# Performance work log

Hardware: AMD Instinct MI355X
Metric: run time of the kernel (lower is better)

## Reference

```python
import jax, jax.numpy as jnp
import numpy as np

N = 50000      # nodes (src = dst at both layers)
E = 800000     # edges per layer
T = 8          # time steps
C_IN = 16      # input channels
HID = 16       # conv1 out channels (hardcoded in SAGENet)
C_OUT = 32     # final out channels


def setup_inputs() -> dict:
    key = jax.random.key(0)
    ks = jax.random.split(key, 10)
    X = jax.random.normal(ks[0], (T, N, C_IN), dtype=jnp.float32)
    edge_index0 = jax.random.randint(ks[1], (2, E), 0, N, dtype=jnp.int32)
    edge_weight0 = jax.random.uniform(ks[2], (E,), dtype=jnp.float32)
    edge_index1 = jax.random.randint(ks[3], (2, E), 0, N, dtype=jnp.int32)
    edge_weight1 = jax.random.uniform(ks[4], (E,), dtype=jnp.float32)
    res_n_id0 = jnp.arange(N, dtype=jnp.int32)
    res_n_id1 = jnp.arange(N, dtype=jnp.int32)
    W1 = jax.random.normal(ks[5], (2 * C_IN, HID), dtype=jnp.float32) * 0.1
    b1 = jax.random.normal(ks[6], (HID,), dtype=jnp.float32) * 0.1
    W2 = jax.random.normal(ks[7], (2 * HID, C_OUT), dtype=jnp.float32) * 0.1
    b2 = jax.random.normal(ks[8], (C_OUT,), dtype=jnp.float32) * 0.1
    return {"X": X, "edge_index0": edge_index0, "edge_weight0": edge_weight0,
            "edge_index1": edge_index1, "edge_weight1": edge_weight1,
            "res_n_id0": res_n_id0, "res_n_id1": res_n_id1,
            "W1": W1, "b1": b1, "W2": W2, "b2": b2}


def sage_conv(x, edge_index, edge_weight, res_n_id, num_dst, W, b):
    # x: [N_src, T, C]; message = edge_weight * x[src]; mean-aggregate to dst;
    # concat residual x[res_n_id] then linear (old PyG SAGEConv, concat=True).
    src, dst = edge_index[0], edge_index[1]
    msg = x[src] * edge_weight[:, None, None]                      # [E, T, C]
    summed = jax.ops.segment_sum(msg, dst, num_segments=num_dst)   # [Nd, T, C]
    cnt = jax.ops.segment_sum(jnp.ones_like(edge_weight), dst, num_segments=num_dst)
    aggr = summed / jnp.maximum(cnt, 1.0)[:, None, None]
    h = jnp.concatenate([x[res_n_id], aggr], axis=-1)              # [Nd, T, 2C]
    return jnp.einsum('ntc,cd->ntd', h, W) + b


def reference(X, edge_index0, edge_weight0, edge_index1, edge_weight1,
              res_n_id0, res_n_id1, W1, b1, W2, b2):
    x = jnp.transpose(X, (1, 0, 2))                                # [N, T, C]
    x = jax.nn.leaky_relu(sage_conv(x, edge_index0, edge_weight0, res_n_id0, N, W1, b1), 0.01)
    x = jax.nn.leaky_relu(sage_conv(x, edge_index1, edge_weight1, res_n_id1, N, W2, b2), 0.01)
    return jnp.transpose(x, (1, 0, 2))                             # [T, N, C_out]
```

## Files before the change

kernel.cpp:

```cpp
#include <hip/hip_runtime.h>
#include <hip/hip_bf16.h>
#include <stdint.h>

static constexpr int Nn   = 50000;
static constexpr int Ee   = 800000;
static constexpr int Tt   = 8;
static constexpr int CIN  = 16;
static constexpr int HID  = 16;
static constexpr int COUT = 32;
static constexpr int TC   = Tt * CIN;
static constexpr int ROWD = TC / 2;

static constexpr int NB  = (2 * Nn + 255) / 256;
static constexpr int CAP = 16;

typedef __attribute__((ext_vector_type(8))) short short8;
typedef __attribute__((ext_vector_type(4))) float f32x4;
union FU { uint4 u4; short8 s8; };

__device__ inline float bflo(uint32_t u) { return __uint_as_float(u << 16); }
__device__ inline float bfhi(uint32_t u) { return __uint_as_float(u & 0xffff0000u); }
__device__ inline unsigned short f2bf(float x) {
    __hip_bfloat16 h = __float2bfloat16(x);
    unsigned short u; __builtin_memcpy(&u, &h, 2); return u;
}
__device__ inline uint32_t bfpack(float a, float b) {
    return (uint32_t)f2bf(a) | ((uint32_t)f2bf(b) << 16);
}
__device__ inline void fma8(float2& a0, float2& a1, float2& a2, float2& a3,
                            float w, uint4 r) {
    a0.x += w * bflo(r.x); a0.y += w * bfhi(r.x);
    a1.x += w * bflo(r.y); a1.y += w * bfhi(r.y);
    a2.x += w * bflo(r.z); a2.y += w * bfhi(r.z);
    a3.x += w * bflo(r.w); a3.y += w * bfhi(r.w);
}
__device__ inline void redg(float2& a) {
    a.x += __shfl_xor(a.x, 16); a.y += __shfl_xor(a.y, 16);
    a.x += __shfl_xor(a.x, 32); a.y += __shfl_xor(a.y, 32);
}

__global__ void k_detect_stage(const unsigned short* __restrict__ x16, int nvals,
                               int* __restrict__ flag,
                               const void* W1, const void* b1,
                               const void* W2, const void* b2,
                               float* __restrict__ biasbuf,
                               uint32_t* __restrict__ wpk1,
                               uint32_t* __restrict__ wpk2,
                               int* __restrict__ bucketCnt) {
    __shared__ int bad;
    int tid = threadIdx.x;
    if (tid == 0) bad = 0;
    __syncthreads();
    for (int i = tid; i < nvals; i += 256) {
        int ex = (x16[i] >> 7) & 0xFF;
        if (ex >= 0x8D) atomicOr(&bad, 1);
    }
    __syncthreads();
    int f = bad;
    if (tid == 0) flag[0] = f;
    auto ldf = [&](const void* srcp, int idx) -> float {
        return f ? ((const float*)srcp)[idx]
                 : __bfloat162float(((const __hip_bfloat16*)srcp)[idx]);
    };
    if (tid < 16) biasbuf[tid] = ldf(b1, tid);
    if (tid >= 16 && tid < 48) biasbuf[tid] = ldf(b2, tid - 16);
    { int h = tid >> 4, d = tid & 15;
      wpk1[tid] = bfpack(ldf(W1, 2 * d * 16 + h), ldf(W1, (2 * d + 1) * 16 + h)); }
    for (int i = tid; i < 512; i += 256) {
        int h = i >> 4, d = i & 15;
        wpk2[i] = bfpack(ldf(W2, 2 * d * 32 + h), ldf(W2, (2 * d + 1) * 32 + h));
    }
    for (int i = tid; i < NB; i += 256) bucketCnt[i] = 0;
}


__global__ __launch_bounds__(256) void k_count(const int* __restrict__ ei0,
                                               const int* __restrict__ ei1,
                                               int* __restrict__ bucketCnt) {
    __shared__ int hist[NB];
    for (int i = threadIdx.x; i < NB; i += 256) hist[i] = 0;
    __syncthreads();
    const int4* d0 = (const int4*)(ei0 + Ee);
    const int4* d1 = (const int4*)(ei1 + Ee);
    int stride = gridDim.x * 256;
    int nq = Ee / 4;
    for (int i = blockIdx.x * 256 + threadIdx.x; i < 2 * nq; i += stride) {
        int4 v; int addn;
        if (i < nq) { v = d0[i]; addn = 0; }
        else        { v = d1[i - nq]; addn = Nn; }
        atomicAdd(&hist[(v.x + addn) >> 8], 1);
        atomicAdd(&hist[(v.y + addn) >> 8], 1);
        atomicAdd(&hist[(v.z + addn) >> 8], 1);
        atomicAdd(&hist[(v.w + addn) >> 8], 1);
    }
    __syncthreads();
    for (int i = threadIdx.x; i < NB; i += 256)
        if (hist[i]) atomicAdd(&bucketCnt[i], hist[i]);
}

__global__ void k_bucketscan(const int* __restrict__ bucketCnt,
                             int* __restrict__ base, int* __restrict__ gcur) {
    __shared__ int tmp[512];
    int tid = threadIdx.x;
    int v = (tid < NB) ? bucketCnt[tid] : 0;
    tmp[tid] = v;
    __syncthreads();
    for (int ofs = 1; ofs < 512; ofs <<= 1) {
        int t = (tid >= ofs) ? tmp[tid - ofs] : 0;
        __syncthreads();
        tmp[tid] += t;
        __syncthreads();
    }
    if (tid < NB) { int b = tmp[tid] - v; base[tid] = b; gcur[tid] = b; }
    if (tid == 0) base[NB] = 2 * Ee;
}

__global__ __launch_bounds__(256) void k_bin(const int* __restrict__ flag,
        const int* __restrict__ ei0, const void* w0v,
        const int* __restrict__ ei1, const void* w1v,
        int* __restrict__ gcur, uint64_t* __restrict__ gout) {
    __shared__ uint64_t rows[NB][CAP];
    __shared__ int cnt[NB];
    int tid = threadIdx.x;
    for (int i = tid; i < NB; i += 256) cnt[i] = 0;
    __syncthreads();
    int f = flag[0];
    int tileStride = gridDim.x * 1024;
    for (int base_e = blockIdx.x * 1024; base_e < 2 * Ee; base_e += tileStride) {
#pragma unroll
        for (int s = 0; s < 4; s++) {
            int e = base_e + s * 256 + tid;
            if (e < 2 * Ee) {
                int g; uint32_t src, wb;
                if (e < Ee) {
                    g = ei0[Ee + e];
                    src = (uint32_t)ei0[e];
                    wb = f ? f2bf(((const float*)w0v)[e])
                           : ((const unsigned short*)w0v)[e];
                } else {
                    int e1 = e - Ee;
                    g = Nn + ei1[Ee + e1];
                    src = (uint32_t)ei1[e1];
                    wb = f ? f2bf(((const float*)w1v)[e1])
                           : ((const unsigned short*)w1v)[e1];
                }
                uint64_t r = ((uint64_t)(uint32_t)g << 32) | (src << 16) | wb;
                int b = g >> 8;
                int idx = atomicAdd(&cnt[b], 1);
                if (idx < CAP) rows[b][idx] = r;
                else { int pos = atomicAdd(&gcur[b], 1); gout[pos] = r; }
            }
        }
        __syncthreads();
        for (int b = tid; b < NB; b += 256) {
            if (cnt[b] >= CAP) {
                int pos = atomicAdd(&gcur[b], CAP);
#pragma unroll
                for (int k = 0; k < CAP; k++) gout[pos + k] = rows[b][k];
                cnt[b] = 0;
            }
        }
        __syncthreads();
    }
    for (int b = tid; b < NB; b += 256) {
        int c = cnt[b];
        if (c > 0) {
            int pos = atomicAdd(&gcur[b], c);
            for (int k = 0; k < c; k++) gout[pos + k] = rows[b][k];
        }
    }
}

__global__ __launch_bounds__(256) void k_csr(const int* __restrict__ base,
        const uint64_t* __restrict__ gout,
        int* __restrict__ off, uint32_t* __restrict__ rec) {
    __shared__ int hist[256];
    __shared__ int tmp[256];
    __shared__ int cur[256];
    __shared__ uint32_t stage[8192];
    int b = blockIdx.x, tid = threadIdx.x;
    int lo = base[b], hi = base[b + 1];
    hist[tid] = 0;
    __syncthreads();
    for (int i = lo + tid; i < hi; i += 256) {
        int gl = (int)(gout[i] >> 32) & 255;
        atomicAdd(&hist[gl], 1);
    }
    __syncthreads();
    int v = hist[tid];
    tmp[tid] = v;
    __syncthreads();
    for (int ofs = 1; ofs < 256; ofs <<= 1) {
        int t = (tid >= ofs) ? tmp[tid - ofs] : 0;
        __syncthreads();
        tmp[tid] += t;
        __syncthreads();
    }
    int excl = tmp[tid] - v;
    int gg = (b << 8) + tid;
    if (gg < 2 * Nn) off[gg] = lo + excl;
    if (b == NB - 1 && tid == 0) off[2 * Nn] = 2 * Ee;
    int count = hi - lo;
    if (count <= 8192) {
        cur[tid] = excl;
        __syncthreads();
        for (int i = lo + tid; i < hi; i += 256) {
            uint64_t r = gout[i];
            int gl = (int)(r >> 32) & 255;
            int pos = atomicAdd(&cur[gl], 1);
            stage[pos] = (uint32_t)r;
        }
        __syncthreads();
        for (int i = tid; i < count; i += 256) rec[lo + i] = stage[i];
    } else {
        cur[tid] = lo + excl;
        __syncthreads();
        for (int i = lo + tid; i < hi; i += 256) {
            uint64_t r = gout[i];
            int gl = (int)(r >> 32) & 255;
            int pos = atomicAdd(&cur[gl], 1);
            rec[pos] = (uint32_t)r;
        }
    }
}

__global__ void k_transpose(const int* __restrict__ flag, const void* Xv,
                            uint32_t* __restrict__ xrows) {
    int f = flag[0];
    int i = blockIdx.x * blockDim.x + threadIdx.x;
    if (i >= Nn * ROWD) return;
    int n = i >> 6;
    int l = i & 63;
    int t = l >> 3;
    int c = (l & 7) * 2;
    int sidx = (t * Nn + n) * CIN + c;
    uint32_t v;
    if (f) {
        float2 ab = ((const float2*)Xv)[sidx >> 1];
        v = bfpack(ab.x, ab.y);
    } else {
        const unsigned short* u = (const unsigned short*)Xv;
        v = (uint32_t)u[sidx] | ((uint32_t)u[sidx + 1] << 16);
    }
    xrows[i] = v;
}


__global__ __launch_bounds__(256) void k_layer1(
    const uint32_t* __restrict__ xrows, const int* __restrict__ off,
    const uint32_t* __restrict__ rec, const int* __restrict__ resid,
    const uint32_t* __restrict__ wpk1, const float* __restrict__ biasbuf,
    uint32_t* __restrict__ h1rows) {
    __shared__ __align__(16) uint32_t shA[32 * 20];
    int tid = threadIdx.x, wv = tid >> 6, lane = tid & 63;
    int g = lane >> 4, p = lane & 15;
    uint4 bfr = ((const uint4*)wpk1)[p * 4 + g];
    float bias = biasbuf[p];
    int n = blockIdx.x * 4 + wv;
    int o0 = __builtin_amdgcn_readfirstlane(off[n]);
    int o1 = __builtin_amdgcn_readfirstlane(off[n + 1]);
    int rn = __builtin_amdgcn_readfirstlane(resid[n]);
    const uint4* xb = (const uint4*)xrows;
    uint4 xs4 = xb[rn * 16 + p];
    float2 a0 = {0.f, 0.f}, a1 = a0, a2 = a0, a3 = a0;
    for (int j = o0; j < o1; j += 8) {
        int j0 = j + g, j1 = j + 4 + g;
        uint32_t e0 = rec[min(j0, o1 - 1)];
        uint32_t e1 = rec[min(j1, o1 - 1)];
        uint4 r0 = xb[(int)(e0 >> 16) * 16 + p];
        uint4 r1 = xb[(int)(e1 >> 16) * 16 + p];
        float w0 = (j0 < o1) ? bflo(e0) : 0.f;
        float w1 = (j1 < o1) ? bflo(e1) : 0.f;
        fma8(a0, a1, a2, a3, w0, r0);
        fma8(a0, a1, a2, a3, w1, r1);
    }
    redg(a0); redg(a1); redg(a2); redg(a3);
    float inv = 1.f / (float)max(o1 - o0, 1);
    uint4 agp;
    agp.x = bfpack(a0.x * inv, a0.y * inv);
    agp.y = bfpack(a1.x * inv, a1.y * inv);
    agp.z = bfpack(a2.x * inv, a2.y * inv);
    agp.w = bfpack(a3.x * inv, a3.y * inv);
    int r = wv * 8 + (p >> 1);
    int hs = (p & 1) * 4;
    if (g == 0)      *(uint4*)&shA[r * 20 + hs] = xs4;
    else if (g == 1) *(uint4*)&shA[r * 20 + 8 + hs] = agp;
    __syncthreads();
    FU fa, fb; fb.u4 = bfr;
    fa.u4 = *(const uint4*)&shA[((wv >> 1) * 16 + p) * 20 + 4 * g];
    f32x4 acc = {bias, bias, bias, bias};
    acc = __builtin_amdgcn_mfma_f32_16x16x32_bf16(fa.s8, fb.s8, acc, 0, 0, 0);
    bool mine = ((g >> 1) == (wv & 1));
#pragma unroll
    for (int rg = 0; rg < 4; rg++) {
        float v = acc[rg];
        v = fmaxf(v, 0.01f * v);
        float vn = __shfl_xor(v, 1);
        if (mine && !(p & 1)) {
            int t = (g & 1) * 4 + rg;
            h1rows[n * 64 + t * 8 + (p >> 1)] = bfpack(v, vn);
        }
    }
}

__global__ __launch_bounds__(256) void k_layer2(
    const int* __restrict__ flag,
    const uint32_t* __restrict__ h1rows, const int* __restrict__ off,
    const uint32_t* __restrict__ rec, const int* __restrict__ resid,
    const uint32_t* __restrict__ wpk2, const float* __restrict__ biasbuf,
    void* __restrict__ outv) {
    __shared__ __align__(16) uint32_t shA[32 * 20];
    int tid = threadIdx.x, wv = tid >> 6, lane = tid & 63;
    int g = lane >> 4, p = lane & 15;
    uint4 b0 = ((const uint4*)wpk2)[p * 4 + g];
    uint4 b1v = ((const uint4*)wpk2)[(p + 16) * 4 + g];
    float bias0 = biasbuf[16 + p];
    float bias1 = biasbuf[32 + p];
    int f = flag[0];
    int n = blockIdx.x * 4 + wv;
    int o0 = __builtin_amdgcn_readfirstlane(off[Nn + n]);
    int o1 = __builtin_amdgcn_readfirstlane(off[Nn + n + 1]);
    int rn = __builtin_amdgcn_readfirstlane(resid[n]);
    const uint4* xb = (const uint4*)h1rows;
    uint4 xs4 = xb[rn * 16 + p];
    float2 a0 = {0.f, 0.f}, a1 = a0, a2 = a0, a3 = a0;
    for (int j = o0; j < o1; j += 8) {
        int j0 = j + g, j1 = j + 4 + g;
        uint32_t e0 = rec[min(j0, o1 - 1)];
        uint32_t e1 = rec[min(j1, o1 - 1)];
        uint4 r0 = xb[(int)(e0 >> 16) * 16 + p];
        uint4 r1 = xb[(int)(e1 >> 16) * 16 + p];
        float w0 = (j0 < o1) ? bflo(e0) : 0.f;
        float w1 = (j1 < o1) ? bflo(e1) : 0.f;
        fma8(a0, a1, a2, a3, w0, r0);
        fma8(a0, a1, a2, a3, w1, r1);
    }
    redg(a0); redg(a1); redg(a2); redg(a3);
    float inv = 1.f / (float)max(o1 - o0, 1);
    uint4 agp;
    agp.x = bfpack(a0.x * inv, a0.y * inv);
    agp.y = bfpack(a1.x * inv, a1.y * inv);
    agp.z = bfpack(a2.x * inv, a2.y * inv);
    agp.w = bfpack(a3.x * inv, a3.y * inv);
    int r = wv * 8 + (p >> 1);
    int hs = (p & 1) * 4;
    if (g == 0)      *(uint4*)&shA[r * 20 + hs] = xs4;
    else if (g == 1) *(uint4*)&shA[r * 20 + 8 + hs] = agp;
    __syncthreads();
    FU fa, fb0, fb1; fb0.u4 = b0; fb1.u4 = b1v;
    fa.u4 = *(const uint4*)&shA[((wv >> 1) * 16 + p) * 20 + 4 * g];
    f32x4 acc0 = {bias0, bias0, bias0, bias0};
    f32x4 acc1 = {bias1, bias1, bias1, bias1};
    acc0 = __builtin_amdgcn_mfma_f32_16x16x32_bf16(fa.s8, fb0.s8, acc0, 0, 0, 0);
    acc1 = __builtin_amdgcn_mfma_f32_16x16x32_bf16(fa.s8, fb1.s8, acc1, 0, 0, 0);
    bool mine = ((g >> 1) == (wv & 1));
    if (mine) {
#pragma unroll
        for (int rg = 0; rg < 4; rg++) {
            int t = (g & 1) * 4 + rg;
            size_t idx = ((size_t)(t * Nn + n)) * COUT + p;
            float v = acc0[rg]; v = fmaxf(v, 0.01f * v);
            float u = acc1[rg]; u = fmaxf(u, 0.01f * u);
            if (f) {
                ((float*)outv)[idx] = v;
                ((float*)outv)[idx + 16] = u;
            } else {
                ((__hip_bfloat16*)outv)[idx] = __float2bfloat16(v);
                ((__hip_bfloat16*)outv)[idx + 16] = __float2bfloat16(u);
            }
        }
    }
}


extern "C" void kernel_launch(void* const* d_in, const int* in_sizes, int n_in,
                              void* d_out, int out_size, void* d_ws, size_t ws_size,
                              hipStream_t stream) {
    const void* X   = d_in[0];
    const int* ei0  = (const int*)d_in[1];
    const void* w0  = d_in[2];
    const int* ei1  = (const int*)d_in[3];
    const void* w1  = d_in[4];
    const int* rn0  = (const int*)d_in[5];
    const int* rn1  = (const int*)d_in[6];
    const void* W1  = d_in[7];
    const void* b1  = d_in[8];
    const void* W2  = d_in[9];
    const void* b2  = d_in[10];

    char* ws = (char*)d_ws;
    size_t p = 0;
    auto alloc = [&](size_t bytes) -> char* {
        p = (p + 255) & ~(size_t)255;
        char* r = ws + p;
        p += bytes;
        return r;
    };
    int* flag        = (int*)alloc(4);
    float* biasbuf   = (float*)alloc(48 * 4);
    uint32_t* wpk1   = (uint32_t*)alloc(256 * 4);
    uint32_t* wpk2   = (uint32_t*)alloc(512 * 4);
    int* bucketCnt   = (int*)alloc(NB * 4);
    int* base        = (int*)alloc((NB + 1) * 4);
    int* gcur        = (int*)alloc(NB * 4);
    int* off         = (int*)alloc(((size_t)2 * Nn + 1) * 4);
    uint32_t* recf   = (uint32_t*)alloc((size_t)2 * Ee * 4);
    uint32_t* h1rows = (uint32_t*)alloc((size_t)Nn * ROWD * 4);
    uint64_t* gout   = (uint64_t*)alloc((size_t)2 * Ee * 8);
    uint32_t* xrows  = (uint32_t*)gout;

    hipLaunchKernelGGL(k_detect_stage, dim3(1), dim3(256), 0, stream,
                       (const unsigned short*)X, 16384, flag, W1, b1, W2, b2,
                       biasbuf, wpk1, wpk2, bucketCnt);
    hipLaunchKernelGGL(k_count, dim3(256), dim3(256), 0, stream,
                       ei0, ei1, bucketCnt);
    hipLaunchKernelGGL(k_bucketscan, dim3(1), dim3(512), 0, stream,
                       bucketCnt, base, gcur);
    hipLaunchKernelGGL(k_bin, dim3(512), dim3(256), 0, stream,
                       flag, ei0, w0, ei1, w1, gcur, gout);
    hipLaunchKernelGGL(k_csr, dim3(NB), dim3(256), 0, stream,
                       base, gout, off, recf);
    hipLaunchKernelGGL(k_transpose, dim3((Nn * ROWD + 255) / 256), dim3(256), 0, stream,
                       flag, X, xrows);
    hipLaunchKernelGGL(k_layer1, dim3(Nn / 4), dim3(256), 0, stream,
                       xrows, off, recf, rn0, wpk1, biasbuf, h1rows);
    hipLaunchKernelGGL(k_layer2, dim3(Nn / 4), dim3(256), 0, stream,
                       flag, h1rows, off, recf, rn1, wpk2, biasbuf, d_out);
    (void)in_sizes; (void)n_in; (void)out_size; (void)ws_size;
}
```

Baseline: 261.1 us.

## Fuse count with detect and transpose with binning; single-pass block binning

```diff
diff --git a/kernel.cpp b/kernel.cpp
--- a/kernel.cpp
+++ b/kernel.cpp
@@ -14,6 +14,10 @@
 static constexpr int NB  = (2 * Nn + 255) / 256;
 static constexpr int CAP = 16;
 
+static constexpr int BINB = 768;
+static constexpr int EPB  = (2 * Ee + BINB - 1) / BINB;
+static constexpr int TRB  = 1536;
+
 typedef __attribute__((ext_vector_type(8))) short short8;
 typedef __attribute__((ext_vector_type(4))) float f32x4;
 union FU { uint4 u4; short8 s8; };
@@ -39,52 +43,48 @@
     a.x += __shfl_xor(a.x, 32); a.y += __shfl_xor(a.y, 32);
 }
 
-__global__ void k_detect_stage(const unsigned short* __restrict__ x16, int nvals,
-                               int* __restrict__ flag,
-                               const void* W1, const void* b1,
-                               const void* W2, const void* b2,
-                               float* __restrict__ biasbuf,
-                               uint32_t* __restrict__ wpk1,
-                               uint32_t* __restrict__ wpk2,
-                               int* __restrict__ bucketCnt) {
-    __shared__ int bad;
+__global__ __launch_bounds__(256) void k_count_detect(
+        const int* __restrict__ ei0, const int* __restrict__ ei1,
+        int* __restrict__ bucketCnt,
+        const unsigned short* __restrict__ x16, int nvals,
+        int* __restrict__ flag,
+        const void* W1, const void* b1, const void* W2, const void* b2,
+        float* __restrict__ biasbuf,
+        uint32_t* __restrict__ wpk1, uint32_t* __restrict__ wpk2) {
     int tid = threadIdx.x;
-    if (tid == 0) bad = 0;
-    __syncthreads();
-    for (int i = tid; i < nvals; i += 256) {
-        int ex = (x16[i] >> 7) & 0xFF;
-        if (ex >= 0x8D) atomicOr(&bad, 1);
-    }
-    __syncthreads();
-    int f = bad;
-    if (tid == 0) flag[0] = f;
-    auto ldf = [&](const void* srcp, int idx) -> float {
-        return f ? ((const float*)srcp)[idx]
-                 : __bfloat162float(((const __hip_bfloat16*)srcp)[idx]);
-    };
-    if (tid < 16) biasbuf[tid] = ldf(b1, tid);
-    if (tid >= 16 && tid < 48) biasbuf[tid] = ldf(b2, tid - 16);
-    { int h = tid >> 4, d = tid & 15;
-      wpk1[tid] = bfpack(ldf(W1, 2 * d * 16 + h), ldf(W1, (2 * d + 1) * 16 + h)); }
-    for (int i = tid; i < 512; i += 256) {
-        int h = i >> 4, d = i & 15;
-        wpk2[i] = bfpack(ldf(W2, 2 * d * 32 + h), ldf(W2, (2 * d + 1) * 32 + h));
-    }
-    for (int i = tid; i < NB; i += 256) bucketCnt[i] = 0;
-}
-
-
-__global__ __launch_bounds__(256) void k_count(const int* __restrict__ ei0,
-                                               const int* __restrict__ ei1,
-                                               int* __restrict__ bucketCnt) {
+    if (blockIdx.x >= 256) {
+        __shared__ int bad;
+        if (tid == 0) bad = 0;
+        __syncthreads();
+        for (int i = tid; i < nvals; i += 256) {
+            int ex = (x16[i] >> 7) & 0xFF;
+            if (ex >= 0x8D) atomicOr(&bad, 1);
+        }
+        __syncthreads();
+        int f = bad;
+        if (tid == 0) flag[0] = f;
+        auto ldf = [&](const void* srcp, int idx) -> float {
+            return f ? ((const float*)srcp)[idx]
+                     : __bfloat162float(((const __hip_bfloat16*)srcp)[idx]);
+        };
+        if (tid < 16) biasbuf[tid] = ldf(b1, tid);
+        if (tid >= 16 && tid < 48) biasbuf[tid] = ldf(b2, tid - 16);
+        { int h = tid >> 4, d = tid & 15;
+          wpk1[tid] = bfpack(ldf(W1, 2 * d * 16 + h), ldf(W1, (2 * d + 1) * 16 + h)); }
+        for (int i = tid; i < 512; i += 256) {
+            int h = i >> 4, d = i & 15;
+            wpk2[i] = bfpack(ldf(W2, 2 * d * 32 + h), ldf(W2, (2 * d + 1) * 32 + h));
+        }
+        return;
+    }
     __shared__ int hist[NB];
-    for (int i = threadIdx.x; i < NB; i += 256) hist[i] = 0;
+    for (int i = tid; i < NB; i += 256) hist[i] = 0;
     __syncthreads();
     const int4* d0 = (const int4*)(ei0 + Ee);
     const int4* d1 = (const int4*)(ei1 + Ee);
-    int stride = gridDim.x * 256;
+    int stride = 256 * 256;
     int nq = Ee / 4;
-    for (int i = blockIdx.x * 256 + threadIdx.x; i < 2 * nq; i += stride) {
+    for (int i = blockIdx.x * 256 + tid; i < 2 * nq; i += stride) {
         int4 v; int addn;
         if (i < nq) { v = d0[i]; addn = 0; }
         else        { v = d1[i - nq]; addn = Nn; }
@@ -94,7 +94,7 @@
         atomicAdd(&hist[(v.w + addn) >> 8], 1);
     }
     __syncthreads();
-    for (int i = threadIdx.x; i < NB; i += 256)
+    for (int i = tid; i < NB; i += 256)
         if (hist[i]) atomicAdd(&bucketCnt[i], hist[i]);
 }
 
@@ -115,59 +115,73 @@
     if (tid == 0) base[NB] = 2 * Ee;
 }
 
-__global__ __launch_bounds__(256) void k_bin(const int* __restrict__ flag,
+__global__ __launch_bounds__(256) void k_bin_tr(const int* __restrict__ flag,
         const int* __restrict__ ei0, const void* w0v,
         const int* __restrict__ ei1, const void* w1v,
-        int* __restrict__ gcur, uint64_t* __restrict__ gout) {
+        int* __restrict__ gcur, uint64_t* __restrict__ gout,
+        const void* Xv, uint32_t* __restrict__ xrows) {
     __shared__ uint64_t rows[NB][CAP];
     __shared__ int cnt[NB];
+    __shared__ int posArr[NB];
     int tid = threadIdx.x;
+    int bid = blockIdx.x;
+    if (bid >= BINB) {
+        int f = flag[0];
+        int stride = TRB * 256;
+        for (int i = (bid - BINB) * 256 + tid; i < Nn * ROWD; i += stride) {
+            int n = i >> 6;
+            int l = i & 63;
+            int t = l >> 3;
+            int c = (l & 7) * 2;
+            int sidx = (t * Nn + n) * CIN + c;
+            uint32_t v;
+            if (f) {
+                float2 ab = ((const float2*)Xv)[sidx >> 1];
+                v = bfpack(ab.x, ab.y);
+            } else {
+                const unsigned short* u = (const unsigned short*)Xv;
+                v = (uint32_t)u[sidx] | ((uint32_t)u[sidx + 1] << 16);
+            }
+            xrows[i] = v;
+        }
+        return;
+    }
     for (int i = tid; i < NB; i += 256) cnt[i] = 0;
     __syncthreads();
     int f = flag[0];
-    int tileStride = gridDim.x * 1024;
-    for (int base_e = blockIdx.x * 1024; base_e < 2 * Ee; base_e += tileStride) {
-#pragma unroll
-        for (int s = 0; s < 4; s++) {
-            int e = base_e + s * 256 + tid;
-            if (e < 2 * Ee) {
-                int g; uint32_t src, wb;
-                if (e < Ee) {
-                    g = ei0[Ee + e];
-                    src = (uint32_t)ei0[e];
-                    wb = f ? f2bf(((const float*)w0v)[e])
-                           : ((const unsigned short*)w0v)[e];
-                } else {
-                    int e1 = e - Ee;
-                    g = Nn + ei1[Ee + e1];
-                    src = (uint32_t)ei1[e1];
-                    wb = f ? f2bf(((const float*)w1v)[e1])
-                           : ((const unsigned short*)w1v)[e1];
-                }
-                uint64_t r = ((uint64_t)(uint32_t)g << 32) | (src << 16) | wb;
-                int b = g >> 8;
-                int idx = atomicAdd(&cnt[b], 1);
-                if (idx < CAP) rows[b][idx] = r;
-                else { int pos = atomicAdd(&gcur[b], 1); gout[pos] = r; }
-            }
-        }
-        __syncthreads();
-        for (int b = tid; b < NB; b += 256) {
-            if (cnt[b] >= CAP) {
-                int pos = atomicAdd(&gcur[b], CAP);
-#pragma unroll
-                for (int k = 0; k < CAP; k++) gout[pos + k] = rows[b][k];
-                cnt[b] = 0;
-            }
-        }
-        __syncthreads();
-    }
+    int lo = bid * EPB;
+    int hi = min(2 * Ee, lo + EPB);
+    for (int e = lo + tid; e < hi; e += 256) {
+        int g; uint32_t src, wb;
+        if (e < Ee) {
+            g = ei0[Ee + e];
+            src = (uint32_t)ei0[e];
+            wb = f ? f2bf(((const float*)w0v)[e])
+                   : ((const unsigned short*)w0v)[e];
+        } else {
+            int e1 = e - Ee;
+            g = Nn + ei1[Ee + e1];
+            src = (uint32_t)ei1[e1];
+            wb = f ? f2bf(((const float*)w1v)[e1])
+                   : ((const unsigned short*)w1v)[e1];
+        }
+        uint64_t r = ((uint64_t)(uint32_t)g << 32) | (src << 16) | wb;
+        int b = g >> 8;
+        int idx = atomicAdd(&cnt[b], 1);
+        if (idx < CAP) rows[b][idx ^ (b & (CAP - 1))] = r;
+        else { int pos = atomicAdd(&gcur[b], 1); gout[pos] = r; }
+    }
+    __syncthreads();
     for (int b = tid; b < NB; b += 256) {
-        int c = cnt[b];
-        if (c > 0) {
-            int pos = atomicAdd(&gcur[b], c);
-            for (int k = 0; k < c; k++) gout[pos + k] = rows[b][k];
-        }
+        int c = min(cnt[b], CAP);
+        posArr[b] = c ? atomicAdd(&gcur[b], c) : 0;
+    }
+    __syncthreads();
+    int wv = tid >> 6, lane = tid & 63;
+    int q = lane >> 4, k = lane & 15;
+    for (int b = wv * 4 + q; b < NB; b += 16) {
+        int c = min(cnt[b], CAP);
+        if (k < c) gout[posArr[b] + k] = rows[b][k ^ (b & (CAP - 1))];
     }
 }
 
@@ -222,27 +236,6 @@
             rec[pos] = (uint32_t)r;
         }
     }
-}
-
-__global__ void k_transpose(const int* __restrict__ flag, const void* Xv,
-                            uint32_t* __restrict__ xrows) {
-    int f = flag[0];
-    int i = blockIdx.x * blockDim.x + threadIdx.x;
-    if (i >= Nn * ROWD) return;
-    int n = i >> 6;
-    int l = i & 63;
-    int t = l >> 3;
-    int c = (l & 7) * 2;
-    int sidx = (t * Nn + n) * CIN + c;
-    uint32_t v;
-    if (f) {
-        float2 ab = ((const float2*)Xv)[sidx >> 1];
-        v = bfpack(ab.x, ab.y);
-    } else {
-        const unsigned short* u = (const unsigned short*)Xv;
-        v = (uint32_t)u[sidx] | ((uint32_t)u[sidx + 1] << 16);
-    }
-    xrows[i] = v;
 }
 
 
@@ -407,21 +400,19 @@
     uint32_t* recf   = (uint32_t*)alloc((size_t)2 * Ee * 4);
     uint32_t* h1rows = (uint32_t*)alloc((size_t)Nn * ROWD * 4);
     uint64_t* gout   = (uint64_t*)alloc((size_t)2 * Ee * 8);
-    uint32_t* xrows  = (uint32_t*)gout;
-
-    hipLaunchKernelGGL(k_detect_stage, dim3(1), dim3(256), 0, stream,
+    uint32_t* xrows  = (uint32_t*)d_out;
+
+    hipMemsetAsync(bucketCnt, 0, NB * sizeof(int), stream);
+    hipLaunchKernelGGL(k_count_detect, dim3(257), dim3(256), 0, stream,
+                       ei0, ei1, bucketCnt,
                        (const unsigned short*)X, 16384, flag, W1, b1, W2, b2,
-                       biasbuf, wpk1, wpk2, bucketCnt);
-    hipLaunchKernelGGL(k_count, dim3(256), dim3(256), 0, stream,
-                       ei0, ei1, bucketCnt);
+                       biasbuf, wpk1, wpk2);
     hipLaunchKernelGGL(k_bucketscan, dim3(1), dim3(512), 0, stream,
                        bucketCnt, base, gcur);
-    hipLaunchKernelGGL(k_bin, dim3(512), dim3(256), 0, stream,
-                       flag, ei0, w0, ei1, w1, gcur, gout);
+    hipLaunchKernelGGL(k_bin_tr, dim3(BINB + TRB), dim3(256), 0, stream,
+                       flag, ei0, w0, ei1, w1, gcur, gout, X, xrows);
     hipLaunchKernelGGL(k_csr, dim3(NB), dim3(256), 0, stream,
                        base, gout, off, recf);
-    hipLaunchKernelGGL(k_transpose, dim3((Nn * ROWD + 255) / 256), dim3(256), 0, stream,
-                       flag, X, xrows);
     hipLaunchKernelGGL(k_layer1, dim3(Nn / 4), dim3(256), 0, stream,
                        xrows, off, recf, rn0, wpk1, biasbuf, h1rows);
     hipLaunchKernelGGL(k_layer2, dim3(Nn / 4), dim3(256), 0, stream,
```

Result: faster. 254.2 us (-2.6%).
